# Kernel tuning notes

Hardware: AMD Instinct MI355X
Metric: run time of the kernel (lower is better)

Reference implementation:

```python
import jax, jax.numpy as jnp
import numpy as np

D_MODEL = 1024
N_HEADS = 16
HEAD_D = D_MODEL // N_HEADS  # d_keys == d_values == 64
B, L = 4, 2048
EPS_CAUSAL = 1e-6


def setup_inputs() -> dict:
    key = jax.random.key(0)
    ks = jax.random.split(key, 11)
    s = 1.0 / np.sqrt(D_MODEL)
    inp = {
        "queries": jax.random.normal(ks[0], (B, L, D_MODEL), jnp.float32),
        "keys": jax.random.normal(ks[1], (B, L, D_MODEL), jnp.float32),
        "values": jax.random.normal(ks[2], (B, L, D_MODEL), jnp.float32),
        # Linear weights stored as [in, out] so y = x @ W + b (same math as torch Linear)
        "Wq": jax.random.uniform(ks[3], (D_MODEL, N_HEADS * HEAD_D), jnp.float32, -s, s),
        "bq": jax.random.uniform(ks[4], (N_HEADS * HEAD_D,), jnp.float32, -s, s),
        "Wk": jax.random.uniform(ks[5], (D_MODEL, N_HEADS * HEAD_D), jnp.float32, -s, s),
        "bk": jax.random.uniform(ks[6], (N_HEADS * HEAD_D,), jnp.float32, -s, s),
        "Wv": jax.random.uniform(ks[7], (D_MODEL, N_HEADS * HEAD_D), jnp.float32, -s, s),
        "bv": jax.random.uniform(ks[8], (N_HEADS * HEAD_D,), jnp.float32, -s, s),
        "Wo": jax.random.uniform(ks[9], (D_MODEL, D_MODEL), jnp.float32, -s, s),
        "bo": jax.random.uniform(ks[10], (D_MODEL,), jnp.float32, -s, s),
    }
    return inp


def _feat(x):
    # feat_proj: elu(x) + 1
    return jax.nn.elu(x) + 1.0


def _causal_linear_attn(qs, ks, vs):
    # qs/ks: [B,L,H,D], vs: [B,L,H,K]; faithful to original (swapped einsum labels,
    # elementwise denominator).
    def step(carry, xs):
        Si, Zi = carry  # Si: [B,H,D,K], Zi: [B,H,D]
        q, k, v = xs    # each [B,H,D]
        Si = Si + jnp.einsum('bhd,bhk->bhdk', k, v)
        Zi = Zi + k
        num = jnp.einsum('bhd,bhkd->bhk', q, Si)      # note label swap, as in source
        Vi = num / (q * Zi + EPS_CAUSAL)               # elementwise denom, as in source
        return (Si, Zi), Vi

    Bn, Ln, H, D = qs.shape
    K = vs.shape[-1]
    Si0 = jnp.zeros((Bn, H, D, K), qs.dtype)
    Zi0 = jnp.zeros((Bn, H, D), qs.dtype)
    xs = (jnp.swapaxes(qs, 0, 1), jnp.swapaxes(ks, 0, 1), jnp.swapaxes(vs, 0, 1))
    _, out = jax.lax.scan(step, (Si0, Zi0), xs)  # out: [L,B,H,K]
    return jnp.swapaxes(out, 0, 1)               # [B,L,H,K]


def reference(queries, keys, values, Wq, bq, Wk, bk, Wv, bv, Wo, bo):
    N, Lq, _ = queries.shape
    H = N_HEADS
    Q = (queries @ Wq + bq).reshape(N, Lq, H, -1)
    Kp = (keys @ Wk + bk).reshape(N, keys.shape[1], H, -1)
    V = (values @ Wv + bv).reshape(N, values.shape[1], H, -1)
    Q_lin = _feat(Q)
    K_lin = _feat(Kp)
    V_lin = _causal_linear_attn(Q_lin, K_lin, V)  # causal=True branch
    new_values = V_lin.reshape(N, Lq, -1)
    return new_values @ Wo + bo
```

## Files before the change

### kernel.cpp

```cpp
#include <hip/hip_runtime.h>
#include <math.h>

#define DM 1024
#define LL 2048
#define BB 4
#define HH 16
#define HD 64
#define CC 64
#define NC (LL / CC)
#define EPSC 1e-6f
#define PS 72

typedef __attribute__((ext_vector_type(8))) short short8;
typedef __attribute__((ext_vector_type(8))) _Float16 half8;
typedef __attribute__((ext_vector_type(4))) float floatx4;

__device__ __forceinline__ float featf(float x) { return x > 0.f ? x + 1.f : __expf(x); }

__device__ __forceinline__ unsigned short f2bf(float f) {
    unsigned int u = __builtin_bit_cast(unsigned int, f);
    u = (u + 0x7FFFu + ((u >> 16) & 1u)) >> 16;
    return (unsigned short)u;
}

__device__ __forceinline__ uint4 cvt8(float4 a, float4 b) {
    uint4 r;
    asm("v_cvt_pk_bf16_f32 %0, %1, %2" : "=v"(r.x) : "v"(a.x), "v"(a.y));
    asm("v_cvt_pk_bf16_f32 %0, %1, %2" : "=v"(r.y) : "v"(a.z), "v"(a.w));
    asm("v_cvt_pk_bf16_f32 %0, %1, %2" : "=v"(r.z) : "v"(b.x), "v"(b.y));
    asm("v_cvt_pk_bf16_f32 %0, %1, %2" : "=v"(r.w) : "v"(b.z), "v"(b.w));
    return r;
}

__device__ __forceinline__ void gload_lds16(const void* g, void* l) {
    __builtin_amdgcn_global_load_lds(
        (const __attribute__((address_space(1))) void*)g,
        (__attribute__((address_space(3))) void*)l,
        16, 0, 0);
}

__device__ __forceinline__ void stage_tile(const void* gp_, int rowstride,
                                           char* lds_base, int tid) {
    const unsigned short* gp = (const unsigned short*)gp_;
#pragma unroll
    for (int m = 0; m < 2; ++m) {
        const int row = m * 32 + (tid >> 3);
        const int g = (tid & 7) ^ (row & 7);
        gload_lds16(gp + (size_t)row * rowstride + g * 8,
                    lds_base + m * 4096 + tid * 16);
    }
}
__device__ __forceinline__ half8 frag_ldh(const char* base, int row, int kc) {
    return *(const half8*)(base + row * 128 + (((kc) ^ (row & 7)) << 4));
}

__global__ __launch_bounds__(256) void transpose4(
    const float* __restrict__ W0, const float* __restrict__ W1,
    const float* __restrict__ W2, const float* __restrict__ W3,
    unsigned short* __restrict__ T0, unsigned short* __restrict__ T1,
    unsigned short* __restrict__ T2, unsigned short* __restrict__ T3)
{
    __shared__ float tile[64][65];
    const int sel = blockIdx.z;
    const float* W = (sel == 0) ? W0 : (sel == 1) ? W1 : (sel == 2) ? W2 : W3;
    unsigned short* Wt = (sel == 0) ? T0 : (sel == 1) ? T1 : (sel == 2) ? T2 : T3;
    const int r0 = blockIdx.y * 64, c0 = blockIdx.x * 64;
    const int tid = threadIdx.x;
#pragma unroll
    for (int e = 0; e < 16; ++e) {
        const int idx = e * 256 + tid;
        const int r = idx >> 6, c = idx & 63;
        tile[r][c] = W[(size_t)(r0 + r) * DM + c0 + c];
    }
    __syncthreads();
#pragma unroll
    for (int e = 0; e < 16; ++e) {
        const int idx = e * 256 + tid;
        const int co = idx >> 6, ro = idx & 63;
        Wt[(size_t)(c0 + co) * DM + r0 + ro] = f2bf(tile[ro][co]);
    }
}

__global__ __launch_bounds__(256) void gemm_qkv(
    const float* __restrict__ Xq, const float* __restrict__ Xk,
    const float* __restrict__ Xv,
    const unsigned short* __restrict__ Wqt, const unsigned short* __restrict__ Wkt,
    const unsigned short* __restrict__ Wvt,
    const float* __restrict__ bq, const float* __restrict__ bk,
    const float* __restrict__ bv,
    _Float16* __restrict__ Qh, _Float16* __restrict__ KTp,
    _Float16* __restrict__ Vh)
{
    __shared__ __align__(16) unsigned short As[128 * 32];
    __shared__ __align__(16) unsigned short Bs[128 * 32];

    const int sel = blockIdx.y;
    const float* Xf = (sel == 0) ? Xq : (sel == 1) ? Xk : Xv;
    const unsigned short* Wt = (sel == 0) ? Wqt : (sel == 1) ? Wkt : Wvt;
    const float* bias = (sel == 0) ? bq : (sel == 1) ? bk : bv;

    const int tid = threadIdx.x;
    const int lane = tid & 63;
    const int w = tid >> 6;
    const int wr = w >> 1, wc = w & 1;
    const int fm = lane & 15;
    const int fq = lane >> 4;
    const int t = (blockIdx.x & 7) * 64 + (blockIdx.x >> 3);
    const int n0 = (t & 7) * 128, m0 = (t >> 3) * 128;

    floatx4 acc[4][4];
#pragma unroll
    for (int i = 0; i < 4; ++i)
#pragma unroll
        for (int j = 0; j < 4; ++j) acc[i][j] = (floatx4){0.f, 0.f, 0.f, 0.f};

    const int row0 = tid >> 2;
    const int row1 = row0 + 64;
    const int slot0 = (tid & 3) ^ (row0 & 3);
    const int slot1 = (tid & 3) ^ (row1 & 3);
    const float* Xa = Xf + (size_t)(m0 + row0) * DM + slot0 * 8;
    const float* Xb = Xf + (size_t)(m0 + row1) * DM + slot1 * 8;
    const unsigned short* Wa = Wt + (size_t)(n0 + row0) * DM + slot0 * 8;
    const unsigned short* Wb = Wt + (size_t)(n0 + row1) * DM + slot1 * 8;

    const int fswz = ((fq ^ (fm & 3)) << 3);

    float4 ra0 = *(const float4*)(Xa);
    float4 ra1 = *(const float4*)(Xa + 4);
    float4 rb0 = *(const float4*)(Xb);
    float4 rb1 = *(const float4*)(Xb + 4);

    for (int k0 = 0; k0 < DM; k0 += 32) {
        gload_lds16(Wa + k0, Bs + (size_t)tid * 8);
        gload_lds16(Wb + k0, Bs + (size_t)(256 + tid) * 8);
        *(uint4*)(As + (size_t)tid * 8) = cvt8(ra0, ra1);
        *(uint4*)(As + (size_t)(256 + tid) * 8) = cvt8(rb0, rb1);
        __syncthreads();

        const int kn = (k0 + 32 < DM) ? (k0 + 32) : 0;
        ra0 = *(const float4*)(Xa + kn);
        ra1 = *(const float4*)(Xa + kn + 4);
        rb0 = *(const float4*)(Xb + kn);
        rb1 = *(const float4*)(Xb + kn + 4);

        short8 af[4], bf[4];
#pragma unroll
        for (int mt = 0; mt < 4; ++mt)
            af[mt] = *(const short8*)(As + (wr * 64 + mt * 16 + fm) * 32 + fswz);
#pragma unroll
        for (int nt = 0; nt < 4; ++nt)
            bf[nt] = *(const short8*)(Bs + (wc * 64 + nt * 16 + fm) * 32 + fswz);
#pragma unroll
        for (int mt = 0; mt < 4; ++mt)
#pragma unroll
            for (int nt = 0; nt < 4; ++nt)
                acc[mt][nt] = __builtin_amdgcn_mfma_f32_16x16x32_bf16(
                    af[mt], bf[nt], acc[mt][nt], 0, 0, 0);

        __builtin_amdgcn_sched_barrier(0);
        __builtin_amdgcn_s_barrier();
        __builtin_amdgcn_sched_barrier(0);
    }

    if (sel != 1) {
        const int act = (sel == 0);
        _Float16* Yh = (sel == 0) ? Qh : Vh;
#pragma unroll
        for (int nt = 0; nt < 4; ++nt) {
            const int col = n0 + wc * 64 + nt * 16 + fm;
            const float bvv = bias[col];
#pragma unroll
            for (int mt = 0; mt < 4; ++mt) {
                const int rbase = m0 + wr * 64 + mt * 16 + fq * 4;
#pragma unroll
                for (int r = 0; r < 4; ++r) {
                    float v = acc[mt][nt][r] + bvv;
                    if (act) v = featf(v);
                    Yh[(size_t)(rbase + r) * DM + col] = (_Float16)v;
                }
            }
        }
    } else {
        const int b = m0 >> 11;
        const int cch = ((m0 & 2047) >> 6) + wr;
        const int h = (n0 >> 6) + wc;
        _Float16* hb = KTp + ((size_t)((b * 16 + h) * 32 + cch)) * 4096;
#pragma unroll
        for (int nt = 0; nt < 4; ++nt) {
            const int j = nt * 16 + fm;
            const float bvv = bias[n0 + wc * 64 + nt * 16 + fm];
#pragma unroll
            for (int mt = 0; mt < 4; ++mt) {
                float o[4];
#pragma unroll
                for (int r = 0; r < 4; ++r)
                    o[r] = featf(acc[mt][nt][r] + bvv);
                union { _Float16 h[4]; uint2 v; } pk;
#pragma unroll
                for (int r = 0; r < 4; ++r) pk.h[r] = (_Float16)o[r];
                *(uint2*)(hb + j * 64 + mt * 16 + fq * 4) = pk.v;
            }
        }
    }
}

__global__ __launch_bounds__(256) void gemm_out(
    const unsigned short* __restrict__ X,
    const unsigned short* __restrict__ Wt,
    const float* __restrict__ bias,
    float* __restrict__ Yf)
{
    __shared__ __align__(16) unsigned short As[128 * 32];
    __shared__ __align__(16) unsigned short Bs[128 * 32];

    const int tid = threadIdx.x;
    const int lane = tid & 63;
    const int w = tid >> 6;
    const int wr = w >> 1, wc = w & 1;
    const int fm = lane & 15;
    const int fq = lane >> 4;
    const int t = (blockIdx.x & 7) * 64 + (blockIdx.x >> 3);
    const int n0 = (t & 7) * 128, m0 = (t >> 3) * 128;

    floatx4 acc[4][4];
#pragma unroll
    for (int i = 0; i < 4; ++i)
#pragma unroll
        for (int j = 0; j < 4; ++j) acc[i][j] = (floatx4){0.f, 0.f, 0.f, 0.f};

    const int row0 = tid >> 2;
    const int row1 = row0 + 64;
    const int slot0 = (tid & 3) ^ (row0 & 3);
    const int slot1 = (tid & 3) ^ (row1 & 3);
    const unsigned short* Xa = X + (size_t)(m0 + row0) * DM + slot0 * 8;
    const unsigned short* Xb = X + (size_t)(m0 + row1) * DM + slot1 * 8;
    const unsigned short* Wa = Wt + (size_t)(n0 + row0) * DM + slot0 * 8;
    const unsigned short* Wb = Wt + (size_t)(n0 + row1) * DM + slot1 * 8;

    const int fswz = ((fq ^ (fm & 3)) << 3);

    for (int k0 = 0; k0 < DM; k0 += 32) {
        gload_lds16(Xa + k0, As + (size_t)tid * 8);
        gload_lds16(Xb + k0, As + (size_t)(256 + tid) * 8);
        gload_lds16(Wa + k0, Bs + (size_t)tid * 8);
        gload_lds16(Wb + k0, Bs + (size_t)(256 + tid) * 8);
        __syncthreads();

        short8 af[4], bf[4];
#pragma unroll
        for (int mt = 0; mt < 4; ++mt)
            af[mt] = *(const short8*)(As + (wr * 64 + mt * 16 + fm) * 32 + fswz);
#pragma unroll
        for (int nt = 0; nt < 4; ++nt)
            bf[nt] = *(const short8*)(Bs + (wc * 64 + nt * 16 + fm) * 32 + fswz);
#pragma unroll
        for (int mt = 0; mt < 4; ++mt)
#pragma unroll
            for (int nt = 0; nt < 4; ++nt)
                acc[mt][nt] = __builtin_amdgcn_mfma_f32_16x16x32_bf16(
                    af[mt], bf[nt], acc[mt][nt], 0, 0, 0);
        __syncthreads();
    }

#pragma unroll
    for (int nt = 0; nt < 4; ++nt) {
        const int col = n0 + wc * 64 + nt * 16 + fm;
        const float bv = bias[col];
#pragma unroll
        for (int mt = 0; mt < 4; ++mt) {
            const int rbase = m0 + wr * 64 + mt * 16 + fq * 4;
#pragma unroll
            for (int r = 0; r < 4; ++r)
                Yf[(size_t)(rbase + r) * DM + col] = acc[mt][nt][r] + bv;
        }
    }
}

__global__ __launch_bounds__(256) void chunk_state(
    const _Float16* __restrict__ KTp, const _Float16* __restrict__ Vp,
    _Float16* __restrict__ Mc, float* __restrict__ Zc)
{
    __shared__ __align__(16) char smem[18432];
    _Float16* VT = (_Float16*)(smem + 8192);
    float* scratch = (float*)(smem + 17408);

    const int blk = blockIdx.x;
    const int bh = blk / NC, c = blk % NC;
    const int b = bh / HH, h = bh % HH;
    const int tid = threadIdx.x;
    const int w = tid >> 6, lane = tid & 63;
    const int fm = lane & 15, fq = lane >> 4;
    const size_t gbase = ((size_t)(b * LL + c * CC)) * DM + h * HD;
    const _Float16* Kblk = KTp + (size_t)blk * 4096;

    stage_tile(Kblk, 64, smem, tid);

    const int lr = tid >> 2, lc0 = (tid & 3) * 16;
    {
        half8 v0 = *(const half8*)(Vp + gbase + (size_t)lr * DM + lc0);
        half8 v1 = *(const half8*)(Vp + gbase + (size_t)lr * DM + lc0 + 8);
        _Float16 va[16];
#pragma unroll
        for (int e = 0; e < 8; ++e) { va[e] = v0[e]; va[8 + e] = v1[e]; }
#pragma unroll
        for (int g = 0; g < 4; ++g)
#pragma unroll
            for (int e0 = 0; e0 < 4; ++e0) {
                const int e = g * 4 + ((e0 + tid) & 3);
                VT[(lc0 + e) * PS + lr] = va[e];
            }
    }
    {
        const int zj = tid & 63, zs = tid >> 6;
        half8 k0 = *(const half8*)(Kblk + zj * 64 + zs * 16);
        half8 k1 = *(const half8*)(Kblk + zj * 64 + zs * 16 + 8);
        float z = 0.f;
#pragma unroll
        for (int e = 0; e < 8; ++e) z += (float)k0[e] + (float)k1[e];
        scratch[zs * 64 + zj] = z;
    }
    __syncthreads();

    if (tid < 64) {
        Zc[(size_t)blk * 64 + tid] = scratch[tid] + scratch[64 + tid] +
                                     scratch[128 + tid] + scratch[192 + tid];
    }

    floatx4 acc[4];
#pragma unroll
    for (int nt = 0; nt < 4; ++nt) acc[nt] = (floatx4){0.f, 0.f, 0.f, 0.f};
    half8 aK[2];
#pragma unroll
    for (int ks = 0; ks < 2; ++ks)
        aK[ks] = frag_ldh(smem, 16 * w + fm, ks * 4 + fq);
#pragma unroll
    for (int nt = 0; nt < 4; ++nt) {
#pragma unroll
        for (int ks = 0; ks < 2; ++ks) {
            half8 bV = *(const half8*)(VT + (nt * 16 + fm) * PS + ks * 32 + fq * 8);
            acc[nt] = __builtin_amdgcn_mfma_f32_16x16x32_f16(aK[ks], bV, acc[nt], 0, 0, 0);
        }
    }
    _Float16* Mout = Mc + (size_t)blk * 4096;
#pragma unroll
    for (int nt = 0; nt < 4; ++nt) {
        const int dv = nt * 16 + fm;
#pragma unroll
        for (int r = 0; r < 4; ++r) {
            const int j = 16 * w + fq * 4 + r;
            Mout[j * 64 + dv] = (_Float16)acc[nt][r];
        }
    }
}

__global__ __launch_bounds__(256) void prefix_state(
    _Float16* __restrict__ Mc, float* __restrict__ Zc)
{
    const int bh = blockIdx.x >> 4;
    const int slice = blockIdx.x & 15;
    const int off = slice * 256 + threadIdx.x;
    float run = 0.f;
    _Float16* p = Mc + (size_t)bh * NC * 4096 + off;
    for (int c = 0; c < NC; ++c) {
        const float v = (float)p[(size_t)c * 4096];
        p[(size_t)c * 4096] = (_Float16)run;
        run += v;
    }
    if (slice == 0 && threadIdx.x < 64) {
        float z = 0.f;
        float* zb = Zc + (size_t)bh * NC * 64 + threadIdx.x;
        for (int c = 0; c < NC; ++c) {
            const float v = zb[c * 64];
            zb[c * 64] = z;
            z += v;
        }
    }
}

#define ATT_Q  0
#define ATT_V  8192
#define ATT_K  16384
#define ATT_M  24576
#define ATT_A  32768
#define ATT_Z  41984
__global__ __launch_bounds__(256) void chunk_attn(
    const _Float16* __restrict__ Qp, const _Float16* __restrict__ Vp,
    const _Float16* __restrict__ KTp, const _Float16* __restrict__ Mtp,
    const float* __restrict__ Zprev, unsigned short* __restrict__ Outb)
{
    __shared__ __align__(16) char smem[50304];
    _Float16* AT = (_Float16*)(smem + ATT_A);
    _Float16* Zf = (_Float16*)(smem + ATT_Z);

    const int blk = blockIdx.x;
    const int bh = blk / NC, c = blk % NC;
    const int b = bh / HH, h = bh % HH;
    const int tid = threadIdx.x;
    const int w = tid >> 6, lane = tid & 63;
    const int fm = lane & 15, fq = lane >> 4;
    const size_t gbase = ((size_t)(b * LL + c * CC)) * DM + h * HD;
    const _Float16* Kblk = KTp + (size_t)blk * 4096;

    stage_tile(Qp + gbase, DM, smem + ATT_Q, tid);
    stage_tile(Vp + gbase, DM, smem + ATT_V, tid);
    stage_tile(Kblk, 64, smem + ATT_K, tid);
    stage_tile(Mtp + (size_t)blk * 4096, 64, smem + ATT_M, tid);

    {
        const int j = lane;
        const _Float16* kr = Kblk + (size_t)j * 64;
        float run = Zprev[(size_t)blk * 64 + j];
        for (int s = 0; s < w; ++s) {
            half8 k0 = *(const half8*)(kr + s * 16);
            half8 k1 = *(const half8*)(kr + s * 16 + 8);
#pragma unroll
            for (int e = 0; e < 8; ++e) run += (float)k0[e] + (float)k1[e];
        }
        half8 k0 = *(const half8*)(kr + w * 16);
        half8 k1 = *(const half8*)(kr + w * 16 + 8);
        float zrow[16];
#pragma unroll
        for (int e = 0; e < 8; ++e) { run += (float)k0[e]; zrow[e] = run; }
#pragma unroll
        for (int e = 0; e < 8; ++e) { run += (float)k1[e]; zrow[8 + e] = run; }
#pragma unroll
        for (int t = 0; t < 16; ++t)
            Zf[(16 * w + t) * 65 + j] = (_Float16)zrow[t];
    }
    __syncthreads();

    half8 qf[2];
#pragma unroll
    for (int ks = 0; ks < 2; ++ks)
        qf[ks] = frag_ldh(smem + ATT_Q, 16 * w + fm, ks * 4 + fq);

    floatx4 acc1[4];
#pragma unroll
    for (int nt = 0; nt < 4; ++nt) acc1[nt] = (floatx4){0.f, 0.f, 0.f, 0.f};
#pragma unroll
    for (int nt = 0; nt < 4; ++nt) {
#pragma unroll
        for (int ks = 0; ks < 2; ++ks) {
            half8 bV = frag_ldh(smem + ATT_V, nt * 16 + fm, ks * 4 + fq);
            acc1[nt] = __builtin_amdgcn_mfma_f32_16x16x32_f16(qf[ks], bV, acc1[nt], 0, 0, 0);
        }
    }

#pragma unroll
    for (int nt = 0; nt < 4; ++nt) {
        const int t = nt * 16 + fm;
#pragma unroll
        for (int r0 = 0; r0 < 4; ++r0) {
            const int r = (r0 + fm) & 3;
            const int i = 16 * w + fq * 4 + r;
            AT[i * PS + t] = (_Float16)((t <= i) ? acc1[nt][r] : 0.f);
        }
    }

    floatx4 acc2[4];
#pragma unroll
    for (int nt = 0; nt < 4; ++nt) acc2[nt] = (floatx4){0.f, 0.f, 0.f, 0.f};
    {
        half8 aA[2];
#pragma unroll
        for (int ks = 0; ks < 2; ++ks)
            aA[ks] = *(const half8*)(AT + (16 * w + fm) * PS + ks * 32 + fq * 8);
#pragma unroll
        for (int nt = 0; nt < 4; ++nt) {
#pragma unroll
            for (int ks = 0; ks < 2; ++ks) {
                half8 bM = frag_ldh(smem + ATT_M, nt * 16 + fm, ks * 4 + fq);
                acc2[nt] = __builtin_amdgcn_mfma_f32_16x16x32_f16(qf[ks], bM, acc2[nt], 0, 0, 0);
            }
#pragma unroll
            for (int ks = 0; ks < 2; ++ks) {
                half8 bK = frag_ldh(smem + ATT_K, nt * 16 + fm, ks * 4 + fq);
                acc2[nt] = __builtin_amdgcn_mfma_f32_16x16x32_f16(aA[ks], bK, acc2[nt], 0, 0, 0);
            }
        }
    }

#pragma unroll
    for (int nt = 0; nt < 4; ++nt) {
        const int j = nt * 16 + fm;
#pragma unroll
        for (int r = 0; r < 4; ++r) {
            const int i = 16 * w + fq * 4 + r;
            const int qoff = i * 128 + (((j >> 3) ^ (i & 7)) << 4) + (j & 7) * 2;
            const float q = (float)(*(const _Float16*)(smem + ATT_Q + qoff));
            const float z = (float)Zf[i * 65 + j];
            const float denom = fmaf(q, z, EPSC);
            Outb[gbase + (size_t)i * DM + j] = f2bf(acc2[nt][r] * __builtin_amdgcn_rcpf(denom));
        }
    }
}

extern "C" void kernel_launch(void* const* d_in, const int* in_sizes, int n_in,
                              void* d_out, int out_size, void* d_ws, size_t ws_size,
                              hipStream_t stream)
{
    (void)in_sizes; (void)n_in; (void)out_size; (void)ws_size;

    const float* queries = (const float*)d_in[0];
    const float* keys    = (const float*)d_in[1];
    const float* values  = (const float*)d_in[2];
    const float* Wq = (const float*)d_in[3];
    const float* bq = (const float*)d_in[4];
    const float* Wk = (const float*)d_in[5];
    const float* bk = (const float*)d_in[6];
    const float* Wv = (const float*)d_in[7];
    const float* bv = (const float*)d_in[8];
    const float* Wo = (const float*)d_in[9];
    const float* bo = (const float*)d_in[10];

    char* ws = (char*)d_ws;
    const size_t MB = 1u << 20;
    unsigned short* Wqt = (unsigned short*)(ws + 48 * MB);
    unsigned short* Wkt = (unsigned short*)(ws + 50 * MB);
    unsigned short* Wvt = (unsigned short*)(ws + 52 * MB);
    unsigned short* Wot = (unsigned short*)(ws + 54 * MB);
    _Float16* Qh  = (_Float16*)(ws + 56 * MB);
    _Float16* Vh  = (_Float16*)(ws + 72 * MB);
    _Float16* KTp = (_Float16*)(ws + 88 * MB);
    _Float16* Mc  = (_Float16*)(ws + 104 * MB);
    float* Zc     = (float*)(ws + 120 * MB);
    unsigned short* attnb = (unsigned short*)(ws + 128 * MB);

    const dim3 gblk(256);

    transpose4<<<dim3(16, 16, 4), gblk, 0, stream>>>(Wq, Wk, Wv, Wo, Wqt, Wkt, Wvt, Wot);

    gemm_qkv<<<dim3(512, 3), gblk, 0, stream>>>(queries, keys, values,
                                                Wqt, Wkt, Wvt, bq, bk, bv,
                                                Qh, KTp, Vh);

    chunk_state<<<dim3(BB * HH * NC), gblk, 0, stream>>>(KTp, Vh, Mc, Zc);
    prefix_state<<<dim3(BB * HH * 16), gblk, 0, stream>>>(Mc, Zc);
    chunk_attn<<<dim3(BB * HH * NC), gblk, 0, stream>>>(Qh, Vh, KTp, Mc, Zc, attnb);

    gemm_out<<<dim3(512), gblk, 0, stream>>>(attnb, Wot, bo, (float*)d_out);
}
```

Before: 321.3 us.

## Double-buffer LDS tiles in QKV and output GEMMs to overlap loads with MFMA

Both projection GEMMs now use two LDS buffers per operand. The next K-tile's global-to-LDS loads (and, in the QKV kernel, the fp32-to-bf16 register staging) are issued before the MFMAs on the current tile, with one barrier per iteration and explicit vmcnt waits. The aim is to hide global memory latency behind matrix compute and cut one of the two barriers per step. The cost is doubled LDS use, which may lower occupancy, and hand-written waitcnt counts that must match the number of outstanding loads exactly.

Measured after the change: 353.2 us. +9.9%, slower.

```diff
diff --git a/kernel.cpp b/kernel.cpp
--- a/kernel.cpp
+++ b/kernel.cpp
@@ -91,8 +91,8 @@
     _Float16* __restrict__ Qh, _Float16* __restrict__ KTp,
     _Float16* __restrict__ Vh)
 {
-    __shared__ __align__(16) unsigned short As[128 * 32];
-    __shared__ __align__(16) unsigned short Bs[128 * 32];
+    __shared__ __align__(16) unsigned short As[2][128 * 32];
+    __shared__ __align__(16) unsigned short Bs[2][128 * 32];
 
     const int sel = blockIdx.y;
     const float* Xf = (sel == 0) ? Xq : (sel == 1) ? Xk : Xv;
@@ -105,8 +105,8 @@
     const int wr = w >> 1, wc = w & 1;
     const int fm = lane & 15;
     const int fq = lane >> 4;
-    const int t = (blockIdx.x & 7) * 64 + (blockIdx.x >> 3);
-    const int n0 = (t & 7) * 128, m0 = (t >> 3) * 128;
+    const int t0_ = (blockIdx.x & 7) * 64 + (blockIdx.x >> 3);
+    const int n0 = (t0_ & 7) * 128, m0 = (t0_ >> 3) * 128;
 
     floatx4 acc[4][4];
 #pragma unroll
@@ -129,27 +129,42 @@
     float4 ra1 = *(const float4*)(Xa + 4);
     float4 rb0 = *(const float4*)(Xb);
     float4 rb1 = *(const float4*)(Xb + 4);
-
-    for (int k0 = 0; k0 < DM; k0 += 32) {
-        gload_lds16(Wa + k0, Bs + (size_t)tid * 8);
-        gload_lds16(Wb + k0, Bs + (size_t)(256 + tid) * 8);
-        *(uint4*)(As + (size_t)tid * 8) = cvt8(ra0, ra1);
-        *(uint4*)(As + (size_t)(256 + tid) * 8) = cvt8(rb0, rb1);
-        __syncthreads();
-
-        const int kn = (k0 + 32 < DM) ? (k0 + 32) : 0;
-        ra0 = *(const float4*)(Xa + kn);
-        ra1 = *(const float4*)(Xa + kn + 4);
-        rb0 = *(const float4*)(Xb + kn);
-        rb1 = *(const float4*)(Xb + kn + 4);
+    gload_lds16(Wa, &Bs[0][(size_t)tid * 8]);
+    gload_lds16(Wb, &Bs[0][(size_t)(256 + tid) * 8]);
+    *(uint4*)(&As[0][(size_t)tid * 8]) = cvt8(ra0, ra1);
+    *(uint4*)(&As[0][(size_t)(256 + tid) * 8]) = cvt8(rb0, rb1);
+    ra0 = *(const float4*)(Xa + 32);
+    ra1 = *(const float4*)(Xa + 36);
+    rb0 = *(const float4*)(Xb + 32);
+    rb1 = *(const float4*)(Xb + 36);
+    __builtin_amdgcn_sched_barrier(0);
+    asm volatile("s_waitcnt vmcnt(4) lgkmcnt(0)" ::: "memory");
+    __builtin_amdgcn_s_barrier();
+    __builtin_amdgcn_sched_barrier(0);
+
+    int cur = 0;
+#pragma unroll 2
+    for (int t = 0; t < 32; ++t) {
+        const int nxt = cur ^ 1;
+        const int kb = ((t + 1) & 31) * 32;
+        const int ka = ((t + 2) & 31) * 32;
+
+        gload_lds16(Wa + kb, &Bs[nxt][(size_t)tid * 8]);
+        gload_lds16(Wb + kb, &Bs[nxt][(size_t)(256 + tid) * 8]);
+        *(uint4*)(&As[nxt][(size_t)tid * 8]) = cvt8(ra0, ra1);
+        *(uint4*)(&As[nxt][(size_t)(256 + tid) * 8]) = cvt8(rb0, rb1);
+        ra0 = *(const float4*)(Xa + ka);
+        ra1 = *(const float4*)(Xa + ka + 4);
+        rb0 = *(const float4*)(Xb + ka);
+        rb1 = *(const float4*)(Xb + ka + 4);
 
         short8 af[4], bf[4];
 #pragma unroll
         for (int mt = 0; mt < 4; ++mt)
-            af[mt] = *(const short8*)(As + (wr * 64 + mt * 16 + fm) * 32 + fswz);
+            af[mt] = *(const short8*)(&As[cur][(wr * 64 + mt * 16 + fm) * 32 + fswz]);
 #pragma unroll
         for (int nt = 0; nt < 4; ++nt)
-            bf[nt] = *(const short8*)(Bs + (wc * 64 + nt * 16 + fm) * 32 + fswz);
+            bf[nt] = *(const short8*)(&Bs[cur][(wc * 64 + nt * 16 + fm) * 32 + fswz]);
 #pragma unroll
         for (int mt = 0; mt < 4; ++mt)
 #pragma unroll
@@ -158,8 +173,10 @@
                     af[mt], bf[nt], acc[mt][nt], 0, 0, 0);
 
         __builtin_amdgcn_sched_barrier(0);
+        asm volatile("s_waitcnt vmcnt(4) lgkmcnt(0)" ::: "memory");
         __builtin_amdgcn_s_barrier();
         __builtin_amdgcn_sched_barrier(0);
+        cur = nxt;
     }
 
     if (sel != 1) {
@@ -210,8 +227,8 @@
     const float* __restrict__ bias,
     float* __restrict__ Yf)
 {
-    __shared__ __align__(16) unsigned short As[128 * 32];
-    __shared__ __align__(16) unsigned short Bs[128 * 32];
+    __shared__ __align__(16) unsigned short As[2][128 * 32];
+    __shared__ __align__(16) unsigned short Bs[2][128 * 32];
 
     const int tid = threadIdx.x;
     const int lane = tid & 63;
@@ -219,8 +236,8 @@
     const int wr = w >> 1, wc = w & 1;
     const int fm = lane & 15;
     const int fq = lane >> 4;
-    const int t = (blockIdx.x & 7) * 64 + (blockIdx.x >> 3);
-    const int n0 = (t & 7) * 128, m0 = (t >> 3) * 128;
+    const int t0_ = (blockIdx.x & 7) * 64 + (blockIdx.x >> 3);
+    const int n0 = (t0_ & 7) * 128, m0 = (t0_ >> 3) * 128;
 
     floatx4 acc[4][4];
 #pragma unroll
@@ -239,27 +256,45 @@
 
     const int fswz = ((fq ^ (fm & 3)) << 3);
 
-    for (int k0 = 0; k0 < DM; k0 += 32) {
-        gload_lds16(Xa + k0, As + (size_t)tid * 8);
-        gload_lds16(Xb + k0, As + (size_t)(256 + tid) * 8);
-        gload_lds16(Wa + k0, Bs + (size_t)tid * 8);
-        gload_lds16(Wb + k0, Bs + (size_t)(256 + tid) * 8);
-        __syncthreads();
+    gload_lds16(Xa, &As[0][(size_t)tid * 8]);
+    gload_lds16(Xb, &As[0][(size_t)(256 + tid) * 8]);
+    gload_lds16(Wa, &Bs[0][(size_t)tid * 8]);
+    gload_lds16(Wb, &Bs[0][(size_t)(256 + tid) * 8]);
+    __builtin_amdgcn_sched_barrier(0);
+    asm volatile("s_waitcnt vmcnt(0)" ::: "memory");
+    __builtin_amdgcn_s_barrier();
+    __builtin_amdgcn_sched_barrier(0);
+
+    int cur = 0;
+#pragma unroll 2
+    for (int t = 0; t < 32; ++t) {
+        const int nxt = cur ^ 1;
+        const int kb = ((t + 1) & 31) * 32;
+
+        gload_lds16(Xa + kb, &As[nxt][(size_t)tid * 8]);
+        gload_lds16(Xb + kb, &As[nxt][(size_t)(256 + tid) * 8]);
+        gload_lds16(Wa + kb, &Bs[nxt][(size_t)tid * 8]);
+        gload_lds16(Wb + kb, &Bs[nxt][(size_t)(256 + tid) * 8]);
 
         short8 af[4], bf[4];
 #pragma unroll
         for (int mt = 0; mt < 4; ++mt)
-            af[mt] = *(const short8*)(As + (wr * 64 + mt * 16 + fm) * 32 + fswz);
+            af[mt] = *(const short8*)(&As[cur][(wr * 64 + mt * 16 + fm) * 32 + fswz]);
 #pragma unroll
         for (int nt = 0; nt < 4; ++nt)
-            bf[nt] = *(const short8*)(Bs + (wc * 64 + nt * 16 + fm) * 32 + fswz);
+            bf[nt] = *(const short8*)(&Bs[cur][(wc * 64 + nt * 16 + fm) * 32 + fswz]);
 #pragma unroll
         for (int mt = 0; mt < 4; ++mt)
 #pragma unroll
             for (int nt = 0; nt < 4; ++nt)
                 acc[mt][nt] = __builtin_amdgcn_mfma_f32_16x16x32_bf16(
                     af[mt], bf[nt], acc[mt][nt], 0, 0, 0);
-        __syncthreads();
+
+        __builtin_amdgcn_sched_barrier(0);
+        asm volatile("s_waitcnt vmcnt(0) lgkmcnt(0)" ::: "memory");
+        __builtin_amdgcn_s_barrier();
+        __builtin_amdgcn_sched_barrier(0);
+        cur = nxt;
     }
 
 #pragma unroll
```

## Pre-convert activations to bf16 in prep kernel and load GEMM A-tiles via LDS DMA

Applied to the files above, without the earlier changes.

Adds a prep kernel that converts the fp32 query/key/value inputs to bf16 in the workspace and folds the weight transposes into the same launch. The QKV GEMM then stages both operands with direct global-to-LDS loads instead of register prefetch plus in-loop conversion. The GEMM grids also switch to plain 2D/3D indexing, dropping the swizzled tile order. This adds an extra full pass over the inputs (read fp32, write bf16) and loses the register prefetch overlap and the L2-friendly block ordering.

Measured after the change: 320.6 us. Within noise of the previous version (-0.2%).

```diff
diff --git a/kernel.cpp b/kernel.cpp
--- a/kernel.cpp
+++ b/kernel.cpp
@@ -54,36 +54,61 @@
     return *(const half8*)(base + row * 128 + (((kc) ^ (row & 7)) << 4));
 }
 
-__global__ __launch_bounds__(256) void transpose4(
+__global__ __launch_bounds__(256) void prep(
+    const float* __restrict__ q, const float* __restrict__ k,
+    const float* __restrict__ v,
     const float* __restrict__ W0, const float* __restrict__ W1,
     const float* __restrict__ W2, const float* __restrict__ W3,
+    unsigned short* __restrict__ qb, unsigned short* __restrict__ kb,
+    unsigned short* __restrict__ vb,
     unsigned short* __restrict__ T0, unsigned short* __restrict__ T1,
     unsigned short* __restrict__ T2, unsigned short* __restrict__ T3)
 {
     __shared__ float tile[64][65];
-    const int sel = blockIdx.z;
-    const float* W = (sel == 0) ? W0 : (sel == 1) ? W1 : (sel == 2) ? W2 : W3;
-    unsigned short* Wt = (sel == 0) ? T0 : (sel == 1) ? T1 : (sel == 2) ? T2 : T3;
-    const int r0 = blockIdx.y * 64, c0 = blockIdx.x * 64;
+    const int bid = blockIdx.x;
     const int tid = threadIdx.x;
-#pragma unroll
-    for (int e = 0; e < 16; ++e) {
-        const int idx = e * 256 + tid;
-        const int r = idx >> 6, c = idx & 63;
-        tile[r][c] = W[(size_t)(r0 + r) * DM + c0 + c];
-    }
-    __syncthreads();
-#pragma unroll
-    for (int e = 0; e < 16; ++e) {
-        const int idx = e * 256 + tid;
-        const int co = idx >> 6, ro = idx & 63;
-        Wt[(size_t)(c0 + co) * DM + r0 + ro] = f2bf(tile[ro][co]);
-    }
-}
-
-__global__ __launch_bounds__(256) void gemm_qkv(
-    const float* __restrict__ Xq, const float* __restrict__ Xk,
-    const float* __restrict__ Xv,
+    if (bid < 1536) {
+        const int sel = bid >> 9;
+        const int ib = bid & 511;
+        const float* src = (sel == 0) ? q : (sel == 1) ? k : v;
+        unsigned short* dst = (sel == 0) ? qb : (sel == 1) ? kb : vb;
+        const size_t u0 = (size_t)ib * 2048 + tid;
+        float4 x[8], y[8];
+#pragma unroll
+        for (int e = 0; e < 8; ++e) {
+            const size_t u = u0 + (size_t)e * 256;
+            x[e] = ((const float4*)src)[u * 2];
+            y[e] = ((const float4*)src)[u * 2 + 1];
+        }
+#pragma unroll
+        for (int e = 0; e < 8; ++e)
+            ((uint4*)dst)[u0 + (size_t)e * 256] = cvt8(x[e], y[e]);
+    } else {
+        const int tb = bid - 1536;
+        const int sel = tb >> 8;
+        const int rem = tb & 255;
+        const float* W = (sel == 0) ? W0 : (sel == 1) ? W1 : (sel == 2) ? W2 : W3;
+        unsigned short* Wt = (sel == 0) ? T0 : (sel == 1) ? T1 : (sel == 2) ? T2 : T3;
+        const int r0 = (rem >> 4) * 64, c0 = (rem & 15) * 64;
+#pragma unroll
+        for (int e = 0; e < 16; ++e) {
+            const int idx = e * 256 + tid;
+            const int r = idx >> 6, c = idx & 63;
+            tile[r][c] = W[(size_t)(r0 + r) * DM + c0 + c];
+        }
+        __syncthreads();
+#pragma unroll
+        for (int e = 0; e < 16; ++e) {
+            const int idx = e * 256 + tid;
+            const int co = idx >> 6, ro = idx & 63;
+            Wt[(size_t)(c0 + co) * DM + r0 + ro] = f2bf(tile[ro][co]);
+        }
+    }
+}
+
+__global__ __launch_bounds__(256) void gemm_qkv3(
+    const unsigned short* __restrict__ qb, const unsigned short* __restrict__ kb,
+    const unsigned short* __restrict__ vb,
     const unsigned short* __restrict__ Wqt, const unsigned short* __restrict__ Wkt,
     const unsigned short* __restrict__ Wvt,
     const float* __restrict__ bq, const float* __restrict__ bk,
@@ -94,8 +119,8 @@
     __shared__ __align__(16) unsigned short As[128 * 32];
     __shared__ __align__(16) unsigned short Bs[128 * 32];
 
-    const int sel = blockIdx.y;
-    const float* Xf = (sel == 0) ? Xq : (sel == 1) ? Xk : Xv;
+    const int sel = blockIdx.z;
+    const unsigned short* X = (sel == 0) ? qb : (sel == 1) ? kb : vb;
     const unsigned short* Wt = (sel == 0) ? Wqt : (sel == 1) ? Wkt : Wvt;
     const float* bias = (sel == 0) ? bq : (sel == 1) ? bk : bv;
 
@@ -105,8 +130,7 @@
     const int wr = w >> 1, wc = w & 1;
     const int fm = lane & 15;
     const int fq = lane >> 4;
-    const int t = (blockIdx.x & 7) * 64 + (blockIdx.x >> 3);
-    const int n0 = (t & 7) * 128, m0 = (t >> 3) * 128;
+    const int m0 = blockIdx.y * 128, n0 = blockIdx.x * 128;
 
     floatx4 acc[4][4];
 #pragma unroll
@@ -118,30 +142,19 @@
     const int row1 = row0 + 64;
     const int slot0 = (tid & 3) ^ (row0 & 3);
     const int slot1 = (tid & 3) ^ (row1 & 3);
-    const float* Xa = Xf + (size_t)(m0 + row0) * DM + slot0 * 8;
-    const float* Xb = Xf + (size_t)(m0 + row1) * DM + slot1 * 8;
+    const unsigned short* Xa = X + (size_t)(m0 + row0) * DM + slot0 * 8;
+    const unsigned short* Xb = X + (size_t)(m0 + row1) * DM + slot1 * 8;
     const unsigned short* Wa = Wt + (size_t)(n0 + row0) * DM + slot0 * 8;
     const unsigned short* Wb = Wt + (size_t)(n0 + row1) * DM + slot1 * 8;
 
     const int fswz = ((fq ^ (fm & 3)) << 3);
 
-    float4 ra0 = *(const float4*)(Xa);
-    float4 ra1 = *(const float4*)(Xa + 4);
-    float4 rb0 = *(const float4*)(Xb);
-    float4 rb1 = *(const float4*)(Xb + 4);
-
     for (int k0 = 0; k0 < DM; k0 += 32) {
+        gload_lds16(Xa + k0, As + (size_t)tid * 8);
+        gload_lds16(Xb + k0, As + (size_t)(256 + tid) * 8);
         gload_lds16(Wa + k0, Bs + (size_t)tid * 8);
         gload_lds16(Wb + k0, Bs + (size_t)(256 + tid) * 8);
-        *(uint4*)(As + (size_t)tid * 8) = cvt8(ra0, ra1);
-        *(uint4*)(As + (size_t)(256 + tid) * 8) = cvt8(rb0, rb1);
         __syncthreads();
-
-        const int kn = (k0 + 32 < DM) ? (k0 + 32) : 0;
-        ra0 = *(const float4*)(Xa + kn);
-        ra1 = *(const float4*)(Xa + kn + 4);
-        rb0 = *(const float4*)(Xb + kn);
-        rb1 = *(const float4*)(Xb + kn + 4);
 
         short8 af[4], bf[4];
 #pragma unroll
@@ -156,10 +169,7 @@
             for (int nt = 0; nt < 4; ++nt)
                 acc[mt][nt] = __builtin_amdgcn_mfma_f32_16x16x32_bf16(
                     af[mt], bf[nt], acc[mt][nt], 0, 0, 0);
-
-        __builtin_amdgcn_sched_barrier(0);
-        __builtin_amdgcn_s_barrier();
-        __builtin_amdgcn_sched_barrier(0);
+        __syncthreads();
     }
 
     if (sel != 1) {
@@ -219,8 +229,7 @@
     const int wr = w >> 1, wc = w & 1;
     const int fm = lane & 15;
     const int fq = lane >> 4;
-    const int t = (blockIdx.x & 7) * 64 + (blockIdx.x >> 3);
-    const int n0 = (t & 7) * 128, m0 = (t >> 3) * 128;
+    const int m0 = blockIdx.y * 128, n0 = blockIdx.x * 128;
 
     floatx4 acc[4][4];
 #pragma unroll
@@ -515,6 +524,9 @@
 
     char* ws = (char*)d_ws;
     const size_t MB = 1u << 20;
+    unsigned short* qb  = (unsigned short*)(ws);
+    unsigned short* kb  = (unsigned short*)(ws + 16 * MB);
+    unsigned short* vb  = (unsigned short*)(ws + 32 * MB);
     unsigned short* Wqt = (unsigned short*)(ws + 48 * MB);
     unsigned short* Wkt = (unsigned short*)(ws + 50 * MB);
     unsigned short* Wvt = (unsigned short*)(ws + 52 * MB);
@@ -528,15 +540,17 @@
 
     const dim3 gblk(256);
 
-    transpose4<<<dim3(16, 16, 4), gblk, 0, stream>>>(Wq, Wk, Wv, Wo, Wqt, Wkt, Wvt, Wot);
-
-    gemm_qkv<<<dim3(512, 3), gblk, 0, stream>>>(queries, keys, values,
-                                                Wqt, Wkt, Wvt, bq, bk, bv,
-                                                Qh, KTp, Vh);
+    prep<<<dim3(2560), gblk, 0, stream>>>(queries, keys, values,
+                                          Wq, Wk, Wv, Wo,
+                                          qb, kb, vb, Wqt, Wkt, Wvt, Wot);
+
+    gemm_qkv3<<<dim3(8, 64, 3), gblk, 0, stream>>>(qb, kb, vb,
+                                                   Wqt, Wkt, Wvt, bq, bk, bv,
+                                                   Qh, KTp, Vh);
 
     chunk_state<<<dim3(BB * HH * NC), gblk, 0, stream>>>(KTp, Vh, Mc, Zc);
     prefix_state<<<dim3(BB * HH * 16), gblk, 0, stream>>>(Mc, Zc);
     chunk_attn<<<dim3(BB * HH * NC), gblk, 0, stream>>>(Qh, Vh, KTp, Mc, Zc, attnb);
 
-    gemm_out<<<dim3(512), gblk, 0, stream>>>(attnb, Wot, bo, (float*)d_out);
-}
+    gemm_out<<<dim3(8, 64), gblk, 0, stream>>>(attnb, Wot, bo, (float*)d_out);
+}
```
